# Optimization experiments

Measured on AMD Instinct MI355X. Metric: run time of the kernel, lower is better.

The kernel has to match this reference:

```python
import jax, jax.numpy as jnp
import numpy as np

NUM_HEADS = 4
DIM_MODEL = 256
DIM_HEAD = DIM_MODEL // NUM_HEADS  # 64


def _conv1x1(w, b, x):
    # Conv1d kernel_size=1: [B, D_in, N] -> [B, D_out, N]
    return jnp.einsum('oi,bin->bon', w, x) + b[None, :, None]


def setup_inputs() -> dict:
    key = jax.random.key(0)
    ks = jax.random.split(key, 12)
    B, D, N = 8, DIM_MODEL, 2048
    s = 1.0 / np.sqrt(D)
    inp = {
        'query': jax.random.normal(ks[0], (B, D, N), dtype=jnp.float32),
        'key': jax.random.normal(ks[1], (B, D, N), dtype=jnp.float32),
        'value': jax.random.normal(ks[2], (B, D, N), dtype=jnp.float32),
        'wq': jax.random.normal(ks[3], (D, D), dtype=jnp.float32) * s,
        'bq': jax.random.normal(ks[4], (D,), dtype=jnp.float32) * 0.01,
        'wk': jax.random.normal(ks[5], (D, D), dtype=jnp.float32) * s,
        'bk': jax.random.normal(ks[6], (D,), dtype=jnp.float32) * 0.01,
        'wv': jax.random.normal(ks[7], (D, D), dtype=jnp.float32) * s,
        'bv': jax.random.normal(ks[8], (D,), dtype=jnp.float32) * 0.01,
        'wm': jax.random.normal(ks[9], (D, D), dtype=jnp.float32) * s,
        'bm': jax.random.normal(ks[10], (D,), dtype=jnp.float32) * 0.01,
    }
    return inp


def reference(query, key, value, wq, bq, wk, bk, wv, bv, wm, bm):
    B = query.shape[0]
    d, h = DIM_HEAD, NUM_HEADS
    # 1x1 conv projections, then split channels as (dim_head, num_heads) per torch view
    q = _conv1x1(wq, bq, query).reshape(B, d, h, -1)  # [B, d, h, N]
    k = _conv1x1(wk, bk, key).reshape(B, d, h, -1)    # [B, d, h, M]
    v = _conv1x1(wv, bv, value).reshape(B, d, h, -1)  # [B, d, h, M]
    norm = 1.0 / float(d) ** 0.5
    scores = jnp.einsum('bdhn,bdhm->bhnm', q, k) * norm  # [B, h, N, M]
    prob = jax.nn.softmax(scores, axis=-1)
    attn = jnp.einsum('bhnm,bdhm->bdhn', prob, v)        # [B, d, h, N]
    out = _conv1x1(wm, bm, attn.reshape(B, d * h, -1))   # [B, D, N]
    return out
```

## Files before the change

kernel.cpp:

```cpp
#include <hip/hip_runtime.h>
#include <math.h>

#define BB 8
#define DD 256
#define NN 2048
#define NH 4
#define DH 64

typedef _Float16 half8   __attribute__((ext_vector_type(8)));
typedef _Float16 half4_t __attribute__((ext_vector_type(4)));
typedef _Float16 half2_t __attribute__((ext_vector_type(2)));
typedef float    floatx4 __attribute__((ext_vector_type(4)));

#define MFMA32(A, B, C) __builtin_amdgcn_mfma_f32_16x16x32_f16(A, B, C, 0, 0, 0)

#define SC 0.18033688011112042f

__global__ __launch_bounds__(256) void prep_weights(
    const float* __restrict__ wq, const float* __restrict__ wk,
    const float* __restrict__ wv, const float* __restrict__ wm,
    _Float16* __restrict__ wqf, _Float16* __restrict__ wkf,
    _Float16* __restrict__ wvf, _Float16* __restrict__ wmf)
{
    int id = blockIdx.x * 256 + threadIdx.x;
    wqf[id] = (_Float16)wq[id];
    wkf[id] = (_Float16)wk[id];
    wvf[id] = (_Float16)wv[id];
    int row = id >> 8, col = id & 255;
    int hh = col >> 6, dd = col & 63;
    wmf[id] = (_Float16)wm[row * 256 + dd * 4 + hh];
}

__global__ __launch_bounds__(256, 3) void conv_qkv(
    const _Float16* __restrict__ wqf, const _Float16* __restrict__ wkf,
    const _Float16* __restrict__ wvf,
    const float* __restrict__ bq, const float* __restrict__ bk,
    const float* __restrict__ bv,
    const float* __restrict__ Xq, const float* __restrict__ Xk,
    const float* __restrict__ Xv,
    _Float16* __restrict__ Yq, _Float16* __restrict__ Yk,
    _Float16* __restrict__ Yv)
{
    const int n0 = blockIdx.x * 64;
    const int b  = blockIdx.y;
    const int z  = blockIdx.z;
    const _Float16* Wf = z == 0 ? wqf : (z == 1 ? wkf : wvf);
    const float* bias  = z == 0 ? bq  : (z == 1 ? bk  : bv);
    const float* X     = z == 0 ? Xq  : (z == 1 ? Xk  : Xv);
    const float osc    = z == 0 ? SC : 1.0f;

    const int t = threadIdx.x;
    const int w = t >> 6, l = t & 63, c = l & 15, q = l >> 4;

    __shared__ _Float16 smem[64 * 264 + 9216];
    _Float16* Xs = smem;
    _Float16* Es = smem + 64 * 264;

    const int gk = (c & 3) << 1;

    {
        const int nb = t & 15, kb = t >> 4;
        const int slot = (kb >> 1), sub = (kb & 1) * 4;
        #pragma unroll
        for (int cc = 0; cc < 4; ++cc) {
            const float* Xg = X + (size_t)b * DD * NN +
                              (size_t)(cc * 64 + kb * 4) * NN + n0 + nb * 4;
            float4 x[4];
            #pragma unroll
            for (int i = 0; i < 4; ++i) x[i] = *(const float4*)(Xg + (size_t)i * NN);
            #pragma unroll
            for (int j = 0; j < 4; ++j) {
                half4_t hv;
                #pragma unroll
                for (int i = 0; i < 4; ++i) hv[i] = (_Float16)(((const float*)&x[i])[j]);
                *(half4_t*)(Xs + (nb * 4 + j) * 264 +
                            (((cc * 8 + slot) ^ (j << 1)) << 3) + sub) = hv;
            }
        }
    }
    __syncthreads();

    for (int hf = 0; hf < 2; ++hf) {
        const int cout0 = hf * 128;

        half8 af[2][8];
        {
            const _Float16* wp = Wf + (size_t)(cout0 + w * 32 + c) * 256 + q * 8;
            #pragma unroll
            for (int rt = 0; rt < 2; ++rt)
                #pragma unroll
                for (int ch = 0; ch < 8; ++ch)
                    af[rt][ch] = *(const half8*)(wp + rt * 16 * 256 + ch * 32);
        }

        floatx4 acc[2][4];
        #pragma unroll
        for (int rt = 0; rt < 2; ++rt)
            #pragma unroll
            for (int nt = 0; nt < 4; ++nt) acc[rt][nt] = (floatx4){0.f, 0.f, 0.f, 0.f};

        #pragma unroll
        for (int ch = 0; ch < 8; ++ch)
            #pragma unroll
            for (int nt = 0; nt < 4; ++nt) {
                half8 bx = *(const half8*)(Xs + (nt * 16 + c) * 264 +
                                           (((ch * 4 + q) ^ gk) << 3));
                acc[0][nt] = MFMA32(af[0][ch], bx, acc[0][nt]);
                acc[1][nt] = MFMA32(af[1][ch], bx, acc[1][nt]);
            }

        if (z < 2) {
            __syncthreads();
            #pragma unroll
            for (int rt = 0; rt < 2; ++rt)
                #pragma unroll
                for (int nt = 0; nt < 4; ++nt) {
                    half4_t hv;
                    #pragma unroll
                    for (int r = 0; r < 4; ++r)
                        hv[r] = (_Float16)((acc[rt][nt][r] +
                                bias[cout0 + w * 32 + rt * 16 + q * 4 + r]) * osc);
                    *(half4_t*)(Es + (nt * 16 + c) * 136 + w * 32 + rt * 16 + q * 4) = hv;
                }
            __syncthreads();
            _Float16* Y = z == 0 ? Yq : Yk;
            const int nn = t >> 2, hh = t & 3;
            half8 hv[4];
            #pragma unroll
            for (int i = 0; i < 4; ++i)
                #pragma unroll
                for (int k = 0; k < 8; ++k)
                    hv[i][k] = Es[nn * 136 + (i * 8 + k) * 4 + hh];
            _Float16* dst = Y + ((size_t)(b * NH + hh) * NN + n0 + nn) * 64 + hf * 32;
            #pragma unroll
            for (int i = 0; i < 4; ++i) *(half8*)(dst + i * 8) = hv[i];
        } else {
            __syncthreads();
            #pragma unroll
            for (int rt = 0; rt < 2; ++rt)
                #pragma unroll
                for (int nt = 0; nt < 4; ++nt)
                    #pragma unroll
                    for (int r = 0; r < 4; ++r)
                        Es[(w * 32 + rt * 16 + q * 4 + r) * 72 + nt * 16 + c] =
                            (_Float16)(acc[rt][nt][r] +
                                       bias[cout0 + w * 32 + rt * 16 + q * 4 + r]);
            __syncthreads();
            const int cl = t >> 1, noff = (t & 1) * 32;
            const int cout = cout0 + cl;
            const int hh = cout & 3, dd = cout >> 2;
            _Float16* dst = Yv + ((size_t)(b * NH + hh) * 64 + dd) * NN + n0 + noff;
            #pragma unroll
            for (int i = 0; i < 4; ++i)
                *(half8*)(dst + i * 8) = *(const half8*)(Es + cl * 72 + noff + i * 8);
        }
    }
}

__global__ __launch_bounds__(256, 3) void conv_o(
    const _Float16* __restrict__ Wf, const float* __restrict__ bias,
    const _Float16* __restrict__ At, float* __restrict__ out)
{
    const int n0 = blockIdx.x * 64;
    const int b  = blockIdx.y;
    const int hf = blockIdx.z;
    const int cout0 = hf * 128;

    const int t = threadIdx.x;
    const int w = t >> 6, l = t & 63, c = l & 15, q = l >> 4;

    __shared__ float fs[128 * 66];

    half8 af[2][8];
    {
        const _Float16* wp = Wf + (size_t)(cout0 + w * 32 + c) * 256 + q * 8;
        #pragma unroll
        for (int rt = 0; rt < 2; ++rt)
            #pragma unroll
            for (int ch = 0; ch < 8; ++ch)
                af[rt][ch] = *(const half8*)(wp + rt * 16 * 256 + ch * 32);
    }

    floatx4 acc[2][4];
    #pragma unroll
    for (int rt = 0; rt < 2; ++rt)
        #pragma unroll
        for (int nt = 0; nt < 4; ++nt) acc[rt][nt] = (floatx4){0.f, 0.f, 0.f, 0.f};

    #pragma unroll
    for (int ch = 0; ch < 8; ++ch)
        #pragma unroll
        for (int nt = 0; nt < 4; ++nt) {
            half8 bx = *(const half8*)(At +
                ((size_t)b * NN + n0 + nt * 16 + c) * 256 + ch * 32 + q * 8);
            acc[0][nt] = MFMA32(af[0][ch], bx, acc[0][nt]);
            acc[1][nt] = MFMA32(af[1][ch], bx, acc[1][nt]);
        }

    #pragma unroll
    for (int rt = 0; rt < 2; ++rt)
        #pragma unroll
        for (int nt = 0; nt < 4; ++nt)
            #pragma unroll
            for (int r = 0; r < 4; ++r)
                fs[(w * 32 + rt * 16 + q * 4 + r) * 66 + nt * 16 + c] =
                    acc[rt][nt][r] + bias[cout0 + w * 32 + rt * 16 + q * 4 + r];
    __syncthreads();
    const int cl = t >> 1, noff = (t & 1) * 32;
    float* dst = out + (size_t)b * DD * NN + (size_t)(cout0 + cl) * NN + n0 + noff;
    #pragma unroll
    for (int i = 0; i < 8; ++i)
        *(float4*)(dst + i * 4) = *(const float4*)(fs + cl * 66 + noff + i * 4);
}

__global__ __launch_bounds__(256, 2) void attn_mfma7(
    const _Float16* __restrict__ Qt, const _Float16* __restrict__ Kt,
    const _Float16* __restrict__ V, _Float16* __restrict__ At)
{
    const int n0 = blockIdx.x * 128;
    const int h  = blockIdx.y;
    const int b  = blockIdx.z;
    const int t  = threadIdx.x;
    const int w  = t >> 6, l = t & 63, c = l & 15, q = l >> 4;

    const size_t bh = (size_t)(b * NH + h);

    __shared__ _Float16 smem[2 * 17920];

    half8 bq2[2][2];
    #pragma unroll
    for (int jj = 0; jj < 2; ++jj)
        #pragma unroll
        for (int ch = 0; ch < 2; ++ch)
            bq2[jj][ch] = *(const half8*)(Qt +
                (bh * NN + n0 + w * 32 + jj * 16 + c) * 64 + ch * 32 + q * 8);

    float lp0 = 0.f, lp1 = 0.f;
    floatx4 o[2][4];
    #pragma unroll
    for (int jj = 0; jj < 2; ++jj)
        #pragma unroll
        for (int dt = 0; dt < 4; ++dt) o[jj][dt] = (floatx4){0.f, 0.f, 0.f, 0.f};

    const int ksr = t >> 1, ksc = (t & 1) * 32;
    const int vr  = t >> 2, vcb = (t & 3) * 32;
    const _Float16* Kg = Kt + bh * NN * 64;
    const _Float16* Vg = V + bh * 64 * NN;

    half8 kpre[4], vpre[4];
    #pragma unroll
    for (int u = 0; u < 4; ++u) {
        kpre[u] = *(const half8*)(Kg + (size_t)ksr * 64 + ksc + u * 8);
        vpre[u] = *(const half8*)(Vg + (size_t)vr * NN + vcb + u * 8);
    }

#define STAGE_TILE(KSP, VSP)                                                    \
    {                                                                           \
        _Pragma("unroll")                                                       \
        for (int u = 0; u < 4; ++u)                                             \
            *(half8*)((KSP) + ksr * 72 + ksc + u * 8) = kpre[u];                \
        _Pragma("unroll")                                                       \
        for (int u = 0; u < 4; ++u) {                                           \
            const int mb = vcb + u * 8;                                         \
            const int p0 = (mb & ~31) + (((mb >> 2) & 3) << 3) +                \
                           (((mb >> 4) & 1) << 2);                              \
            half4_t lo, hi;                                                     \
            _Pragma("unroll")                                                   \
            for (int j = 0; j < 4; ++j) { lo[j] = vpre[u][j]; hi[j] = vpre[u][4 + j]; } \
            *(half4_t*)((VSP) + vr * 136 + p0)     = lo;                        \
            *(half4_t*)((VSP) + vr * 136 + p0 + 8) = hi;                        \
        }                                                                       \
    }

    STAGE_TILE(smem, smem + 9216);
    #pragma unroll
    for (int u = 0; u < 4; ++u) {
        kpre[u] = *(const half8*)(Kg + (size_t)(128 + ksr) * 64 + ksc + u * 8);
        vpre[u] = *(const half8*)(Vg + (size_t)vr * NN + 128 + vcb + u * 8);
    }
    __syncthreads();

    for (int it = 0; it < 16; ++it) {
        if (it < 15) {
            _Float16* Ksw = smem + ((it + 1) & 1) * 17920;
            STAGE_TILE(Ksw, Ksw + 9216);
        }
        {
            const int mn = (it + 2 < 16) ? (it + 2) * 128 : it * 128;
            #pragma unroll
            for (int u = 0; u < 4; ++u) {
                kpre[u] = *(const half8*)(Kg + (size_t)(mn + ksr) * 64 + ksc + u * 8);
                vpre[u] = *(const half8*)(Vg + (size_t)vr * NN + mn + vcb + u * 8);
            }
        }
        const _Float16* Ks = smem + (it & 1) * 17920;
        const _Float16* Vs = Ks + 9216;
        #pragma unroll
        for (int mt2 = 0; mt2 < 4; ++mt2) {
            half8 p8[2];
            #pragma unroll
            for (int hfm = 0; hfm < 2; ++hfm) {
                const int mt = mt2 * 2 + hfm;
                half8 ak0 = *(const half8*)(Ks + (mt * 16 + c) * 72 + q * 8);
                half8 ak1 = *(const half8*)(Ks + (mt * 16 + c) * 72 + 32 + q * 8);
                #pragma unroll
                for (int jj = 0; jj < 2; ++jj) {
                    floatx4 s = {0.f, 0.f, 0.f, 0.f};
                    s = MFMA32(ak0, bq2[jj][0], s);
                    s = MFMA32(ak1, bq2[jj][1], s);
                    float e0 = exp2f(s[0]), e1 = exp2f(s[1]);
                    float e2 = exp2f(s[2]), e3 = exp2f(s[3]);
                    if (jj == 0) lp0 += (e0 + e1) + (e2 + e3);
                    else         lp1 += (e0 + e1) + (e2 + e3);
                    half2_t c01 = __builtin_bit_cast(half2_t, __builtin_amdgcn_cvt_pkrtz(e0, e1));
                    half2_t c23 = __builtin_bit_cast(half2_t, __builtin_amdgcn_cvt_pkrtz(e2, e3));
                    p8[jj][hfm * 4 + 0] = c01[0]; p8[jj][hfm * 4 + 1] = c01[1];
                    p8[jj][hfm * 4 + 2] = c23[0]; p8[jj][hfm * 4 + 3] = c23[1];
                }
            }
            #pragma unroll
            for (int dt = 0; dt < 4; ++dt) {
                half8 av = *(const half8*)(Vs + (dt * 16 + c) * 136 + mt2 * 32 + q * 8);
                o[0][dt] = MFMA32(av, p8[0], o[0][dt]);
                o[1][dt] = MFMA32(av, p8[1], o[1][dt]);
            }
        }
        __syncthreads();
    }
#undef STAGE_TILE

    lp0 += __shfl_xor(lp0, 16); lp0 += __shfl_xor(lp0, 32);
    lp1 += __shfl_xor(lp1, 16); lp1 += __shfl_xor(lp1, 32);
    const float inv0 = 1.f / lp0, inv1 = 1.f / lp1;

    _Float16* fsm = smem;
    #pragma unroll
    for (int jj = 0; jj < 2; ++jj) {
        const float inv = jj == 0 ? inv0 : inv1;
        #pragma unroll
        for (int dt = 0; dt < 4; ++dt) {
            half4_t hv;
            #pragma unroll
            for (int r = 0; r < 4; ++r) hv[r] = (_Float16)(o[jj][dt][r] * inv);
            *(half4_t*)(fsm + (w * 32 + jj * 16 + c) * 72 + dt * 16 + q * 4) = hv;
        }
    }
    __syncthreads();
    #pragma unroll
    for (int rr = 0; rr < 2; ++rr) {
        const int rn = rr * 64 + (t >> 2), seg = (t & 3) * 16;
        _Float16* dst = At + ((size_t)b * NN + n0 + rn) * 256 + h * 64 + seg;
        *(half8*)(dst)     = *(const half8*)(fsm + rn * 72 + seg);
        *(half8*)(dst + 8) = *(const half8*)(fsm + rn * 72 + seg + 8);
    }
}

extern "C" void kernel_launch(void* const* d_in, const int* in_sizes, int n_in,
                              void* d_out, int out_size, void* d_ws, size_t ws_size,
                              hipStream_t stream) {
    const float* query = (const float*)d_in[0];
    const float* key_  = (const float*)d_in[1];
    const float* value = (const float*)d_in[2];
    const float* wq    = (const float*)d_in[3];
    const float* bq    = (const float*)d_in[4];
    const float* wk    = (const float*)d_in[5];
    const float* bk    = (const float*)d_in[6];
    const float* wv    = (const float*)d_in[7];
    const float* bv    = (const float*)d_in[8];
    const float* wm    = (const float*)d_in[9];
    const float* bm    = (const float*)d_in[10];
    float* out = (float*)d_out;

    _Float16* ws = (_Float16*)d_ws;
    _Float16* wqf = ws;
    _Float16* wkf = wqf + 65536;
    _Float16* wvf = wkf + 65536;
    _Float16* wmf = wvf + 65536;
    const size_t e16 = (size_t)BB * NH * NN * DH;
    _Float16* qf = ws + 262144;
    _Float16* kf = qf + e16;
    _Float16* vf = kf + e16;
    _Float16* at = vf + e16;

    prep_weights<<<256, 256, 0, stream>>>(wq, wk, wv, wm, wqf, wkf, wvf, wmf);
    conv_qkv<<<dim3(32, 8, 3), 256, 0, stream>>>(wqf, wkf, wvf, bq, bk, bv,
                                                 query, key_, value, qf, kf, vf);
    attn_mfma7<<<dim3(16, 4, 8), 256, 0, stream>>>(qf, kf, vf, at);
    conv_o<<<dim3(32, 8, 2), 256, 0, stream>>>(wmf, bm, at, out);
}
```

Before: 202.1 us.

## Split attention key range across two wave groups per block and merge partials

```diff
diff --git a/kernel.cpp b/kernel.cpp
--- a/kernel.cpp
+++ b/kernel.cpp
@@ -213,7 +213,7 @@
         *(float4*)(dst + i * 4) = *(const float4*)(fs + cl * 66 + noff + i * 4);
 }
 
-__global__ __launch_bounds__(256, 2) void attn_mfma7(
+__global__ __launch_bounds__(512, 4) void attn_mfma8(
     const _Float16* __restrict__ Qt, const _Float16* __restrict__ Kt,
     const _Float16* __restrict__ V, _Float16* __restrict__ At)
 {
@@ -222,10 +222,14 @@
     const int b  = blockIdx.z;
     const int t  = threadIdx.x;
     const int w  = t >> 6, l = t & 63, c = l & 15, q = l >> 4;
+    const int mh = w >> 2;
+    const int w4 = w & 3;
+    const int tp = t & 255;
 
     const size_t bh = (size_t)(b * NH + h);
 
-    __shared__ _Float16 smem[2 * 17920];
+    __shared__ _Float16 smem[36864];
+    _Float16* base = smem + mh * 18432;
 
     half8 bq2[2][2];
     #pragma unroll
@@ -233,7 +237,7 @@
         #pragma unroll
         for (int ch = 0; ch < 2; ++ch)
             bq2[jj][ch] = *(const half8*)(Qt +
-                (bh * NN + n0 + w * 32 + jj * 16 + c) * 64 + ch * 32 + q * 8);
+                (bh * NN + n0 + w4 * 32 + jj * 16 + c) * 64 + ch * 32 + q * 8);
 
     float lp0 = 0.f, lp1 = 0.f;
     floatx4 o[2][4];
@@ -242,61 +246,59 @@
         #pragma unroll
         for (int dt = 0; dt < 4; ++dt) o[jj][dt] = (floatx4){0.f, 0.f, 0.f, 0.f};
 
-    const int ksr = t >> 1, ksc = (t & 1) * 32;
-    const int vr  = t >> 2, vcb = (t & 3) * 32;
-    const _Float16* Kg = Kt + bh * NN * 64;
-    const _Float16* Vg = V + bh * 64 * NN;
-
-    half8 kpre[4], vpre[4];
-    #pragma unroll
-    for (int u = 0; u < 4; ++u) {
+    const int ksr = tp >> 2, ksc = (tp & 3) * 16;
+    const int vr  = tp >> 2, vcb = (tp & 3) * 16;
+    const _Float16* Kg = Kt + bh * NN * 64 + (size_t)mh * 1024 * 64;
+    const _Float16* Vg = V + bh * 64 * NN + mh * 1024;
+
+    half8 kpre[2], vpre[2];
+    #pragma unroll
+    for (int u = 0; u < 2; ++u) {
         kpre[u] = *(const half8*)(Kg + (size_t)ksr * 64 + ksc + u * 8);
         vpre[u] = *(const half8*)(Vg + (size_t)vr * NN + vcb + u * 8);
     }
 
-#define STAGE_TILE(KSP, VSP)                                                    \
+#define STAGE8(BUFP)                                                            \
     {                                                                           \
+        _Float16* Ksp_ = (BUFP);                                                \
+        *(half8*)(Ksp_ + ksr * 72 + ksc)     = kpre[0];                         \
+        *(half8*)(Ksp_ + ksr * 72 + ksc + 8) = kpre[1];                         \
+        _Float16* Vsp_ = (BUFP) + 4608;                                         \
         _Pragma("unroll")                                                       \
-        for (int u = 0; u < 4; ++u)                                             \
-            *(half8*)((KSP) + ksr * 72 + ksc + u * 8) = kpre[u];                \
-        _Pragma("unroll")                                                       \
-        for (int u = 0; u < 4; ++u) {                                           \
+        for (int u = 0; u < 2; ++u) {                                           \
             const int mb = vcb + u * 8;                                         \
             const int p0 = (mb & ~31) + (((mb >> 2) & 3) << 3) +                \
                            (((mb >> 4) & 1) << 2);                              \
             half4_t lo, hi;                                                     \
             _Pragma("unroll")                                                   \
             for (int j = 0; j < 4; ++j) { lo[j] = vpre[u][j]; hi[j] = vpre[u][4 + j]; } \
-            *(half4_t*)((VSP) + vr * 136 + p0)     = lo;                        \
-            *(half4_t*)((VSP) + vr * 136 + p0 + 8) = hi;                        \
+            *(half4_t*)(Vsp_ + vr * 72 + p0)     = lo;                          \
+            *(half4_t*)(Vsp_ + vr * 72 + p0 + 8) = hi;                          \
         }                                                                       \
     }
 
-    STAGE_TILE(smem, smem + 9216);
-    #pragma unroll
-    for (int u = 0; u < 4; ++u) {
-        kpre[u] = *(const half8*)(Kg + (size_t)(128 + ksr) * 64 + ksc + u * 8);
-        vpre[u] = *(const half8*)(Vg + (size_t)vr * NN + 128 + vcb + u * 8);
+    STAGE8(base);
+    #pragma unroll
+    for (int u = 0; u < 2; ++u) {
+        kpre[u] = *(const half8*)(Kg + (size_t)(64 + ksr) * 64 + ksc + u * 8);
+        vpre[u] = *(const half8*)(Vg + (size_t)vr * NN + 64 + vcb + u * 8);
     }
     __syncthreads();
 
     for (int it = 0; it < 16; ++it) {
-        if (it < 15) {
-            _Float16* Ksw = smem + ((it + 1) & 1) * 17920;
-            STAGE_TILE(Ksw, Ksw + 9216);
-        }
+        if (it < 15) STAGE8(base + ((it + 1) & 1) * 9216);
         {
-            const int mn = (it + 2 < 16) ? (it + 2) * 128 : it * 128;
-            #pragma unroll
-            for (int u = 0; u < 4; ++u) {
+            const int mn = (it + 2 < 16) ? (it + 2) * 64 : it * 64;
+            #pragma unroll
+            for (int u = 0; u < 2; ++u) {
                 kpre[u] = *(const half8*)(Kg + (size_t)(mn + ksr) * 64 + ksc + u * 8);
                 vpre[u] = *(const half8*)(Vg + (size_t)vr * NN + mn + vcb + u * 8);
             }
         }
-        const _Float16* Ks = smem + (it & 1) * 17920;
-        const _Float16* Vs = Ks + 9216;
-        #pragma unroll
-        for (int mt2 = 0; mt2 < 4; ++mt2) {
+        const _Float16* Ks = base + (it & 1) * 9216;
+        const _Float16* Vs = Ks + 4608;
+        #pragma unroll
+        for (int mt2 = 0; mt2 < 2; ++mt2) {
             half8 p8[2];
             #pragma unroll
             for (int hfm = 0; hfm < 2; ++hfm) {
@@ -320,38 +322,64 @@
             }
             #pragma unroll
             for (int dt = 0; dt < 4; ++dt) {
-                half8 av = *(const half8*)(Vs + (dt * 16 + c) * 136 + mt2 * 32 + q * 8);
+                half8 av = *(const half8*)(Vs + (dt * 16 + c) * 72 + mt2 * 32 + q * 8);
                 o[0][dt] = MFMA32(av, p8[0], o[0][dt]);
                 o[1][dt] = MFMA32(av, p8[1], o[1][dt]);
             }
         }
         __syncthreads();
     }
-#undef STAGE_TILE
+#undef STAGE8
 
     lp0 += __shfl_xor(lp0, 16); lp0 += __shfl_xor(lp0, 32);
     lp1 += __shfl_xor(lp1, 16); lp1 += __shfl_xor(lp1, 32);
-    const float inv0 = 1.f / lp0, inv1 = 1.f / lp1;
-
-    _Float16* fsm = smem;
-    #pragma unroll
-    for (int jj = 0; jj < 2; ++jj) {
-        const float inv = jj == 0 ? inv0 : inv1;
-        #pragma unroll
-        for (int dt = 0; dt < 4; ++dt) {
-            half4_t hv;
-            #pragma unroll
-            for (int r = 0; r < 4; ++r) hv[r] = (_Float16)(o[jj][dt][r] * inv);
-            *(half4_t*)(fsm + (w * 32 + jj * 16 + c) * 72 + dt * 16 + q * 4) = hv;
+
+    float* fo = (float*)smem;
+    float* lq = (float*)smem + 128 * 68;
+    _Float16* fsm = (_Float16*)(lq + 128);
+
+    if (mh == 1) {
+        #pragma unroll
+        for (int jj = 0; jj < 2; ++jj) {
+            const int col = w4 * 32 + jj * 16 + c;
+            #pragma unroll
+            for (int dt = 0; dt < 4; ++dt)
+                #pragma unroll
+                for (int r = 0; r < 4; ++r)
+                    fo[col * 68 + dt * 16 + q * 4 + r] = o[jj][dt][r];
+        }
+        if (l < 16) {
+            lq[w4 * 32 + c]      = lp0;
+            lq[w4 * 32 + 16 + c] = lp1;
         }
     }
     __syncthreads();
-    #pragma unroll
-    for (int rr = 0; rr < 2; ++rr) {
-        const int rn = rr * 64 + (t >> 2), seg = (t & 3) * 16;
-        _Float16* dst = At + ((size_t)b * NN + n0 + rn) * 256 + h * 64 + seg;
-        *(half8*)(dst)     = *(const half8*)(fsm + rn * 72 + seg);
-        *(half8*)(dst + 8) = *(const half8*)(fsm + rn * 72 + seg + 8);
+    if (mh == 0) {
+        #pragma unroll
+        for (int jj = 0; jj < 2; ++jj) {
+            const int col = w4 * 32 + jj * 16 + c;
+            const float lpt = (jj == 0 ? lp0 : lp1) + lq[col];
+            const float inv = 1.f / lpt;
+            #pragma unroll
+            for (int dt = 0; dt < 4; ++dt) {
+                half4_t hv;
+                #pragma unroll
+                for (int r = 0; r < 4; ++r)
+                    hv[r] = (_Float16)((o[jj][dt][r] +
+                                        fo[col * 68 + dt * 16 + q * 4 + r]) * inv);
+                *(half4_t*)(fsm + col * 72 + dt * 16 + q * 4) = hv;
+            }
+        }
+    }
+    __syncthreads();
+    if (t < 256) {
+        #pragma unroll
+        for (int rr = 0; rr < 2; ++rr) {
+            const int rn = rr * 64 + (t >> 2), seg = (t & 3) * 16;
+            _Float16* dst = At + ((size_t)b * NN + n0 + rn) * 256 + h * 64 + seg;
+            *(half8*)(dst)     = *(const half8*)(fsm + rn * 72 + seg);
+            *(half8*)(dst + 8) = *(const half8*)(fsm + rn * 72 + seg + 8);
+        }
     }
 }
 
@@ -385,6 +413,6 @@
     prep_weights<<<256, 256, 0, stream>>>(wq, wk, wv, wm, wqf, wkf, wvf, wmf);
     conv_qkv<<<dim3(32, 8, 3), 256, 0, stream>>>(wqf, wkf, wvf, bq, bk, bv,
                                                  query, key_, value, qf, kf, vf);
-    attn_mfma7<<<dim3(16, 4, 8), 256, 0, stream>>>(qf, kf, vf, at);
+    attn_mfma8<<<dim3(16, 4, 8), 512, 0, stream>>>(qf, kf, vf, at);
     conv_o<<<dim3(32, 8, 2), 256, 0, stream>>>(wmf, bm, at, out);
 }
```

Result: faster. 195.1 us (-3.5%).
